# Kernel optimization log

Hardware: AMD Instinct MI355X
Metric: run time of the kernel (lower is better)

Reference implementation:

```python
import jax, jax.numpy as jnp
from jax import lax
import numpy as np

B, T = 8, 16
IMG = 128
CF = 32            # c_CNN_out = dim_C2_2 (feature channels / NTM slot width)
WO = HO = 32       # w_CNN_out, h_CNN_out
N = WO * HO        # dim_C2_1 = NTM memory slots (flattened spatial)
M = CF
DH = 256           # dim_h_o
LAMBDA0 = 1e-4
EPS = 1e-8


def setup_inputs() -> dict:
    key = jax.random.key(0)
    ks = jax.random.split(key, 12)
    f32 = jnp.float32
    inp = {}
    inp["x_i"] = jax.random.normal(ks[0], (B, T, 3, IMG, IMG), f32)
    inp["z_i"] = jax.random.normal(ks[1], (B, T, 3, IMG, IMG), f32)
    # feature CNN (3 -> CF -> CF, stride 2 each)
    inp["conv1_w"] = jax.random.normal(ks[2], (CF, 3, 3, 3), f32) * 0.1
    inp["conv1_b"] = jnp.zeros((CF,), f32)
    inp["conv2_w"] = jax.random.normal(ks[3], (CF, CF, 3, 3), f32) * 0.05
    inp["conv2_b"] = jnp.zeros((CF,), f32)
    # NTM controller / addressing parameters
    inp["Wk"] = jax.random.normal(ks[4], (M, DH), f32) * 0.05
    inp["bk"] = jnp.zeros((M,), f32)
    inp["Wbeta"] = jax.random.normal(ks[5], (1, DH), f32) * 0.05
    inp["bbeta"] = jnp.zeros((1,), f32)
    inp["Wh"] = jax.random.normal(ks[6], (DH, DH + 2 * M), f32) * 0.05
    inp["bh"] = jnp.zeros((DH,), f32)
    inp["We"] = jax.random.normal(ks[7], (M, DH), f32) * 0.05
    inp["Wa"] = jax.random.normal(ks[8], (M, DH), f32) * 0.05
    inp["Wg"] = jax.random.normal(ks[9], (1, DH), f32) * 0.05
    # DCF cosine window and gaussian-label FFT (stored as real/imag pair like torch.rfft)
    win = np.hanning(WO)
    inp["cos_window"] = jnp.asarray(np.outer(win, win), f32)
    sigma = 2.0
    g = np.arange(WO)
    g = np.minimum(g, WO - g)  # circular distance, peak at origin
    d2 = g[:, None] ** 2 + g[None, :] ** 2
    y = np.exp(-d2 / (2.0 * sigma ** 2)).astype(np.float32)
    yfc = np.fft.rfft2(y)
    inp["yf"] = jnp.asarray(np.stack([yfc.real, yfc.imag], -1), f32)[None, None]  # [1,1,WO,WO//2+1,2]
    return inp


def _conv(x, w, b):
    out = lax.conv_general_dilated(x, w, (2, 2), "SAME",
                                   dimension_numbers=("NCHW", "OIHW", "NCHW"))
    return out + b[None, :, None, None]


def _feature(x, c1w, c1b, c2w, c2b):
    x = jax.nn.relu(_conv(x, c1w, c1b))
    return jax.nn.relu(_conv(x, c2w, c2b))  # [BT, CF, WO, HO]


def _layernorm(x):
    # LayerNorm over last two dims [dim_C2_1, dim_C2_2], no affine
    mu = x.mean(axis=(-2, -1), keepdims=True)
    var = x.var(axis=(-2, -1), keepdims=True)
    return (x - mu) / jnp.sqrt(var + 1e-5)


def reference(x_i, z_i, conv1_w, conv1_b, conv2_w, conv2_b,
              Wk, bk, Wbeta, bbeta, Wh, bh, We, Wa, Wg, cos_window, yf):
    # feature extraction
    xf_btcwh = _feature(x_i.reshape(B * T, 3, IMG, IMG), conv1_w, conv1_b, conv2_w, conv2_b)
    zf_btcwh = _feature(z_i.reshape(B * T, 3, IMG, IMG), conv1_w, conv1_b, conv2_w, conv2_b)
    xf = xf_btcwh.transpose(0, 2, 3, 1).reshape(B, T, N, M)  # [B,T,N,M]

    h0 = jnp.zeros((B, DH), xf.dtype)
    c0 = _layernorm(xf[:, 0])  # init_x_norm on first frame features

    def cell(carry, x_t):
        h, c = carry  # h [B,DH], c [B,N,M]; x_t [B,N,M]
        # content-based addressing
        k = jnp.tanh(h @ Wk.T + bk)                           # [B,M]
        beta = jax.nn.softplus(h @ Wbeta.T + bbeta)           # [B,1]
        cn = c / (jnp.linalg.norm(c, axis=-1, keepdims=True) + EPS)
        kn = k / (jnp.linalg.norm(k, axis=-1, keepdims=True) + EPS)
        sims = jnp.einsum("bnm,bm->bn", cn, kn)               # cosine sim [B,N]
        w = jax.nn.softmax(beta * sims, axis=-1)              # read/write weights
        r = jnp.einsum("bn,bnm->bm", w, c)                    # read vector
        # controller update
        inp = jnp.concatenate([h, r, x_t.mean(axis=1)], axis=-1)  # [B,DH+2M]
        h_new = jnp.tanh(inp @ Wh.T + bh)
        # erase / add / input-gate write
        e = jax.nn.sigmoid(h_new @ We.T)                      # [B,M]
        a = jnp.tanh(h_new @ Wa.T)                            # [B,M]
        g = jax.nn.sigmoid(h_new @ Wg.T)[:, :, None]          # [B,1,1]
        c_write = c * (1.0 - w[:, :, None] * e[:, None, :]) + w[:, :, None] * a[:, None, :]
        c_new = (1.0 - g) * c_write + g * x_t
        return (h_new, c_new), c_new

    (_, _), c_seq = lax.scan(cell, (h0, c0), xf.transpose(1, 0, 2, 3))
    c_seq = c_seq.transpose(1, 0, 2, 3)                       # [B,T,N,M]

    # c.permute(0,1,3,2).view(B*T, dim_C2_2, WO, HO)
    c_btcwh = c_seq.transpose(0, 1, 3, 2).reshape(B * T, M, WO, HO)

    # DCF correlation in Fourier domain
    cw = cos_window[None, None]
    cfft = jnp.fft.rfft2(c_btcwh * cw)                        # [BT,M,WO,WO//2+1]
    zfft = jnp.fft.rfft2(zf_btcwh * cw)
    kzzf = (cfft.real ** 2 + cfft.imag ** 2).sum(axis=1, keepdims=True)   # [BT,1,WO,Wf]
    kxzf = (zfft * jnp.conj(cfft)).sum(axis=1, keepdims=True)             # complex_mulconj sum
    yfc = yf[..., 0] + 1j * yf[..., 1]                         # [1,1,WO,Wf]
    alphaf = yfc / (kzzf + LAMBDA0)
    response = jnp.fft.irfft2(kxzf * alphaf, s=(WO, HO))       # [BT,1,WO,HO]
    return response.reshape(B, T, WO, HO)
```

## Files before the change

kernel.cpp:

```cpp
#include <hip/hip_runtime.h>
#include <hip/hip_fp16.h>
#include <math.h>


#define TWOPI_32 0.19634954084936207f

typedef _Float16 __h2 __attribute__((ext_vector_type(2)));
__device__ __forceinline__ float fdot2(unsigned int w, unsigned int h, float acc) {
    union { unsigned int u; __h2 v; } a, b;
    a.u = w; b.u = h;
    return __builtin_amdgcn_fdot2(a.v, b.v, acc, false);
}
__device__ __forceinline__ unsigned int packh2(float a, float b) {
    __half2 h2 = __floats2half2_rn(a, b);
    return *(unsigned int*)&h2;
}

__global__ __launch_bounds__(256) void prepack_kernel(
    const float* __restrict__ Wh, const float* __restrict__ Wk,
    const float* __restrict__ We, const float* __restrict__ Wa,
    const float* __restrict__ c1w, const float* __restrict__ c2w,
    __half* __restrict__ whhP, __half* __restrict__ whrxP,
    __half* __restrict__ wkP, __half* __restrict__ weP, __half* __restrict__ waP,
    float* __restrict__ twg,
    unsigned int* __restrict__ c2wP, unsigned int* __restrict__ c1wP01,
    float* __restrict__ c1wP2)
{
    const int tid = threadIdx.x;
    if (blockIdx.x < 32) {
        const int base = blockIdx.x*256 + tid;
        #pragma unroll
        for (int r = 0; r < 8; ++r) {
            int idx = base*8 + r;
            int e = idx & 7, i = (idx >> 3) & 255, c = idx >> 11;
            int q = c >> 4, k = c & 15;
            whhP[idx] = __float2half(Wh[i*320 + q*128 + k*8 + e]);
        }
        #pragma unroll
        for (int r = 0; r < 2; ++r) {
            int idx = base*2 + r;
            int i = idx >> 6, s2 = idx & 63;
            whrxP[idx] = __float2half(Wh[i*320 + 256 + s2]);
        }
        {
            int idx = base;
            int m = idx >> 8, j = (idx >> 4) & 15, e = idx & 15;
            int col = (e < 8) ? (8*j + e) : (128 + 8*j + (e - 8));
            wkP[idx] = __float2half(Wk[m*256 + col]);
            weP[idx] = __float2half(We[m*256 + col]);
            waP[idx] = __float2half(Wa[m*256 + col]);
        }
    } else {
        for (int idx = tid; idx < 4608; idx += 256) {
            int half = idx / 2304;
            int rem  = idx - half*2304;
            int ic2  = rem / 144;
            int r2   = rem - ic2*144;
            int j    = r2 / 9, q = r2 - j*9;
            int oc   = half*16 + j;
            c2wP[((half*16 + ic2)*16 + j)*12 + q] =
                packh2(c2w[oc*288 + (2*ic2)*9 + q],
                       c2w[oc*288 + (2*ic2+1)*9 + q]);
        }
        for (int idx = tid; idx < 288; idx += 256) {
            int oc = idx / 9, r = idx - oc*9;
            c1wP01[idx] = packh2(c1w[oc*27 + r*3 + 0], c1w[oc*27 + r*3 + 1]);
            c1wP2[idx]  = c1w[oc*27 + r*3 + 2];
        }
        for (int idx = tid; idx < 1024; idx += 256) {
            int w = idx >> 5, k = idx & 31;
            float sv, cv;
            sincosf(TWOPI_32 * (float)((w*k) & 31), &sv, &cv);
            twg[idx*2]     = cv;
            twg[idx*2 + 1] = -sv;
        }
    }
}

__global__ __launch_bounds__(512, 2) void convx_kernel(
    const float* __restrict__ x_i, const unsigned int* __restrict__ c1w01,
    const float* __restrict__ c1w2, const float* __restrict__ c1b,
    const unsigned int* __restrict__ c2wP, const float* __restrict__ c2b,
    float* __restrict__ xfeat, __half* __restrict__ xh, float* __restrict__ xmp)
{
    __shared__ __align__(16) char smem[139264];
    const int team = threadIdx.x >> 8;
    const int t256 = threadIdx.x & 255;
    const int tile = blockIdx.x*2 + team;
    const int img  = tile >> 3;
    const int strip = tile & 7;
    unsigned int* sZ  = (unsigned int*)(smem + team*53072);
    unsigned int* sC1 = (unsigned int*)(smem + team*53072 + 15048);
    unsigned int* sW   = (unsigned int*)(smem + 106144);
    unsigned int* sw01 = (unsigned int*)(smem + 130720);
    float*        sw2  = (float*)(smem + 131872);
    float*        sb2  = (float*)(smem + 133024);
    float*        sb1  = (float*)(smem + 133152);

    for (int i = threadIdx.x; i < 1536; i += 512)
        ((uint4*)sW)[i] = ((const uint4*)c2wP)[i];
    for (int i = threadIdx.x; i < 288; i += 512) { sw01[i] = c1w01[i]; sw2[i] = c1w2[i]; }
    if (threadIdx.x < 32) { sb2[threadIdx.x] = c2b[threadIdx.x]; sb1[threadIdx.x] = c1b[threadIdx.x]; }

    const int zrow0 = strip*16;
    for (int idx = t256; idx < 3762; idx += 256) {
        int ic = idx / (19*66);
        int rem = idx - ic*(19*66);
        int li = rem / 66;
        int x2 = rem - li*66;
        int iy = zrow0 + li;
        unsigned int v = 0;
        if (iy < 128 && x2 < 64) {
            float2 p = *(const float2*)&x_i[(((size_t)img*3 + ic)*128 + iy)*128 + 2*x2];
            v = packh2(p.x, p.y);
        }
        sZ[idx] = v;
    }
    for (int idx = t256; idx < 16*9*2; idx += 256) {
        int oc2 = idx / 18; int rem = idx - oc2*18; int li = rem >> 1; int c = 64 + (rem & 1);
        sC1[oc2*(9*66) + li*66 + c] = 0;
    }
    __syncthreads();
    for (int pos = t256; pos < 576; pos += 256) {
        int li = pos >> 6;
        int ox = pos & 63;
        unsigned int pa[9]; float px[9];
        #pragma unroll
        for (int ic = 0; ic < 3; ++ic)
            #pragma unroll
            for (int dy = 0; dy < 3; ++dy) {
                int r = ic*3 + dy;
                int rowb = ic*(19*66) + (2*li + dy)*66;
                pa[r] = sZ[rowb + ox];
                unsigned int u = sZ[rowb + ox + 1];
                px[r] = __half2float(((const __half2*)&u)->x);
            }
        const bool phantom = (strip == 7) && (li == 8);
        #pragma unroll 4
        for (int oc2 = 0; oc2 < 16; ++oc2) {
            const int oca = 2*oc2, ocb = oca + 1;
            float acca = sb1[oca], accb = sb1[ocb];
            #pragma unroll
            for (int r = 0; r < 9; ++r) {
                acca = fdot2(sw01[oca*9 + r], pa[r], acca);
                acca += sw2[oca*9 + r] * px[r];
                accb = fdot2(sw01[ocb*9 + r], pa[r], accb);
                accb += sw2[ocb*9 + r] * px[r];
            }
            sC1[oc2*(9*66) + li*66 + ox] =
                phantom ? 0u : packh2(fmaxf(acca, 0.f), fmaxf(accb, 0.f));
        }
    }
    __syncthreads();
    const int posl = t256 & 127;
    const int half = t256 >> 7;
    const int ly = posl >> 5;
    const int ox = posl & 31;
    float acc[16];
    #pragma unroll
    for (int j = 0; j < 16; ++j) acc[j] = 0.f;
    for (int ic2 = 0; ic2 < 16; ++ic2) {
        unsigned int patch[9];
        #pragma unroll
        for (int dy = 0; dy < 3; ++dy)
            #pragma unroll
            for (int dx = 0; dx < 3; ++dx)
                patch[dy*3+dx] = sC1[ic2*(9*66) + (2*ly+dy)*66 + 2*ox + dx];
        const unsigned int* wbase = sW + (half*16 + ic2)*192;
        #pragma unroll
        for (int j = 0; j < 16; ++j) {
            const unsigned int* wr = wbase + j*12;
            uint4 wa = *(const uint4*)wr;
            uint4 wb = *(const uint4*)(wr + 4);
            unsigned int w8 = wr[8];
            float a = acc[j];
            a = fdot2(wa.x, patch[0], a); a = fdot2(wa.y, patch[1], a);
            a = fdot2(wa.z, patch[2], a); a = fdot2(wa.w, patch[3], a);
            a = fdot2(wb.x, patch[4], a); a = fdot2(wb.y, patch[5], a);
            a = fdot2(wb.z, patch[6], a); a = fdot2(wb.w, patch[7], a);
            a = fdot2(w8,  patch[8], a);
            acc[j] = a;
        }
    }
    const int oy = strip*4 + ly;
    const int n  = oy*32 + ox;
    float vals[16];
    #pragma unroll
    for (int j = 0; j < 16; ++j) {
        int oc = half*16 + j;
        float v = fmaxf(acc[j] + sb2[oc], 0.f);
        vals[j] = v;
        xfeat[(((size_t)img*32 + oc)*32 + oy)*32 + ox] = v;
    }
    {
        unsigned int hp[8];
        #pragma unroll
        for (int k = 0; k < 8; ++k) hp[k] = packh2(vals[2*k], vals[2*k+1]);
        uint4* dp = (uint4*)(xh + (size_t)img*32768 + (size_t)n*32 + half*16);
        dp[0] = *(uint4*)&hp[0];
        dp[1] = *(uint4*)&hp[4];
    }
    {
        const int lane = threadIdx.x & 63;
        const int wsub = (t256 >> 6) & 1;
        #pragma unroll
        for (int j = 0; j < 16; ++j) {
            float v = vals[j];
            #pragma unroll
            for (int d = 32; d > 0; d >>= 1) v += __shfl_xor(v, d, 64);
            if (lane == 0)
                xmp[(((size_t)img*8 + strip)*2 + wsub)*32 + half*16 + j] = v * (1.f/1024.f);
        }
    }
}

__global__ __launch_bounds__(512, 2) void fat_kernel(
    const float* __restrict__ xfeat, const __half* __restrict__ xh,
    const float* __restrict__ xmp,
    const __half* __restrict__ whhP, const __half* __restrict__ whrxP,
    const __half* __restrict__ wkP, const __half* __restrict__ weP,
    const __half* __restrict__ waP,
    const float* __restrict__ bk, const float* __restrict__ Wbeta,
    const float* __restrict__ bbeta, const float* __restrict__ bh,
    const float* __restrict__ Wg,
    float* __restrict__ wbuf, float* __restrict__ eag, float* __restrict__ lnst,
    const float* __restrict__ z_i, const unsigned int* __restrict__ c1w01,
    const float* __restrict__ c1w2, const float* __restrict__ c1b,
    const unsigned int* __restrict__ c2wP, const float* __restrict__ c2b,
    float* __restrict__ zfeat)
{
    __shared__ __align__(16) char smem[139264];

    if (blockIdx.x < 8) {
        __builtin_amdgcn_s_setprio(1);
        __half* sWhh = (__half*)(smem);
        float (*sHbuf)[256] = (float(*)[256])(smem + 131072);
        __half (*sHh)[256] = (__half(*)[256])(smem + 133120);
        float* sK    = (float*)(smem + 134144);
        float* sXm   = (float*)(smem + 134272);
        float* sRedC = (float*)(smem + 136320);
        float* sR32  = (float*)(smem + 137344);
        float* sE    = (float*)(smem + 137472);
        float* sA    = (float*)(smem + 137600);
        float* sBk   = (float*)(smem + 137728);
        float* sBh   = (float*)(smem + 137856);
        float* sRedD = (float*)(smem + 138880);
        float* sRedL = (float*)(smem + 138912);

        const int b    = blockIdx.x;
        const int tid  = threadIdx.x;
        const int lane = tid & 63;
        const int wid  = tid >> 6;

        {
            const uint4* src = (const uint4*)whhP;
            uint4* dst = (uint4*)sWhh;
            for (int i2 = tid; i2 < 8192; i2 += 512) dst[i2] = src[i2];
        }
        if (tid < 256) { sBh[tid] = bh[tid]; sHbuf[0][tid] = 0.f; sHh[0][tid] = __float2half(0.f); }
        if (tid < 32)  { sBk[tid] = bk[tid]; sK[tid] = tanhf(bk[tid]); }
        if (tid < 512) {
            const int tt = tid >> 5, m = tid & 31;
            const float* pp = xmp + ((size_t)(b*16 + tt)*16)*32 + m;
            float s = 0.f;
            #pragma unroll
            for (int q = 0; q < 16; ++q) s += pp[q*32];
            sXm[tid] = s;
        }
        float4 wbeta4 = *(const float4*)&Wbeta[(size_t)lane*4];
        float4 wg4    = *(const float4*)&Wg[(size_t)lane*4];
        float bb = bbeta[0];

        const int mg = tid >> 4, jg = tid & 15;
        uint4 wk0, wk1, we0, we1, wa0, wa1;
        {
            const uint4* p;
            p = (const uint4*)(wkP + (size_t)(mg*16 + jg)*16); wk0 = p[0]; wk1 = p[1];
            p = (const uint4*)(weP + (size_t)(mg*16 + jg)*16); we0 = p[0]; we1 = p[1];
            p = (const uint4*)(waP + (size_t)(mg*16 + jg)*16); wa0 = p[0]; wa1 = p[1];
        }
        const int iD = tid >> 1, qD = tid & 1;
        uint4 wrx0, wrx1, wrx2, wrx3;
        {
            const uint4* p = (const uint4*)(whrxP + (size_t)iD*64 + qD*32);
            wrx0 = p[0]; wrx1 = p[1]; wrx2 = p[2]; wrx3 = p[3];
        }

        const int n0 = 2*tid;
        float c0[32], c1[32];

        {
            const float* x0 = xfeat + (size_t)(b*16)*32768;
            float sum = 0.f, ss = 0.f;
            #pragma unroll
            for (int m = 0; m < 32; ++m) {
                float2 v = *(const float2*)&x0[m*1024 + n0];
                c0[m] = v.x; c1[m] = v.y;
                sum += v.x + v.y; ss += v.x*v.x + v.y*v.y;
            }
            #pragma unroll
            for (int d = 32; d > 0; d >>= 1) { sum += __shfl_xor(sum, d, 64); ss += __shfl_xor(ss, d, 64); }
            if (lane == 0) { sRedL[wid] = sum; sRedL[8+wid] = ss; }
            __syncthreads();
            float S = 0.f, SS = 0.f;
            #pragma unroll
            for (int i = 0; i < 8; ++i) { S += sRedL[i]; SS += sRedL[8+i]; }
            float mu = S * (1.f/32768.f);
            float var = SS * (1.f/32768.f) - mu*mu;
            float rs = rsqrtf(var + 1e-5f);
            if (tid == 0) { lnst[b*2] = mu; lnst[b*2+1] = rs; }
            #pragma unroll
            for (int m = 0; m < 32; ++m) { c0[m] = (c0[m]-mu)*rs; c1[m] = (c1[m]-mu)*rs; }
        }

        uint4 xb[8];
        {
            const uint4* xrow = (const uint4*)(xh + (size_t)(b*16)*32768) + 8*tid;
            #pragma unroll
            for (int i = 0; i < 8; ++i) xb[i] = xrow[i];
        }
        __syncthreads();

        float betav = (bb > 20.f) ? bb : log1pf(expf(bb));
        float ex0 = 0.f, ex1 = 0.f, w0 = 0.f, w1 = 0.f;
        const int rm = ((lane&1)<<4)|((lane&2)<<2)|(lane&4)|((lane&8)>>2)|((lane&16)>>4);

        #pragma unroll 1
        for (int t = 0; t < 16; ++t) {
            const int cur = t & 1, nxt = cur ^ 1;

            {
                float beta = betav;
                float dot0 = 0.f, dot1 = 0.f, cn20 = 0.f, cn21 = 0.f, kn2 = 0.f;
                #pragma unroll
                for (int q = 0; q < 8; ++q) {
                    float4 k4 = *(const float4*)&sK[4*q];
                    dot0 += c0[4*q]*k4.x + c0[4*q+1]*k4.y + c0[4*q+2]*k4.z + c0[4*q+3]*k4.w;
                    dot1 += c1[4*q]*k4.x + c1[4*q+1]*k4.y + c1[4*q+2]*k4.z + c1[4*q+3]*k4.w;
                    cn20 += c0[4*q]*c0[4*q] + c0[4*q+1]*c0[4*q+1] + c0[4*q+2]*c0[4*q+2] + c0[4*q+3]*c0[4*q+3];
                    cn21 += c1[4*q]*c1[4*q] + c1[4*q+1]*c1[4*q+1] + c1[4*q+2]*c1[4*q+2] + c1[4*q+3]*c1[4*q+3];
                    kn2  += k4.x*k4.x + k4.y*k4.y + k4.z*k4.z + k4.w*k4.w;
                }
                float kinv = 1.f / (sqrtf(kn2) + 1e-8f);
                float s0 = dot0 * kinv / (sqrtf(cn20) + 1e-8f);
                float s1 = dot1 * kinv / (sqrtf(cn21) + 1e-8f);
                ex0 = expf(beta * s0);
                ex1 = expf(beta * s1);
                float es = ex0 + ex1;
                #pragma unroll
                for (int d = 32; d > 0; d >>= 1) es += __shfl_xor(es, d, 64);
                if (lane == 0) sRedD[wid] = es;
                float v[32];
                #pragma unroll
                for (int m = 0; m < 32; ++m) v[m] = ex0*c0[m] + ex1*c1[m];
                #pragma unroll
                for (int i = 0; i < 16; ++i) { float sd = (lane&1)? v[i] : v[i+16]; float rc = __shfl_xor(sd, 1, 64); v[i] = ((lane&1)? v[i+16] : v[i]) + rc; }
                #pragma unroll
                for (int i = 0; i < 8; ++i)  { float sd = (lane&2)? v[i] : v[i+8];  float rc = __shfl_xor(sd, 2, 64); v[i] = ((lane&2)? v[i+8]  : v[i]) + rc; }
                #pragma unroll
                for (int i = 0; i < 4; ++i)  { float sd = (lane&4)? v[i] : v[i+4];  float rc = __shfl_xor(sd, 4, 64); v[i] = ((lane&4)? v[i+4]  : v[i]) + rc; }
                #pragma unroll
                for (int i = 0; i < 2; ++i)  { float sd = (lane&8)? v[i] : v[i+2];  float rc = __shfl_xor(sd, 8, 64); v[i] = ((lane&8)? v[i+2]  : v[i]) + rc; }
                { float sd = (lane&16)? v[0] : v[1]; float rc = __shfl_xor(sd, 16, 64); v[0] = ((lane&16)? v[1] : v[0]) + rc; }
                v[0] += __shfl_xor(v[0], 32, 64);
                if (lane < 32) sRedC[wid*32 + rm] = v[0];
            }
            __syncthreads();

            {
                float den = sRedD[0]+sRedD[1]+sRedD[2]+sRedD[3]+sRedD[4]+sRedD[5]+sRedD[6]+sRedD[7];
                float inv = 1.f / den;
                w0 = ex0 * inv; w1 = ex1 * inv;
                *(float2*)&wbuf[(size_t)(b*16 + t)*1024 + n0] = make_float2(w0, w1);
                if (lane < 32) {
                    float r = 0.f;
                    #pragma unroll
                    for (int w = 0; w < 8; ++w) r += sRedC[w*32 + lane];
                    sR32[lane] = r * inv;
                }
                float s0 = 0.f, s1 = 0.f, s2 = 0.f, s3 = 0.f;
                #pragma unroll
                for (int k4 = 0; k4 < 4; ++k4) {
                    const int kb = 4*k4;
                    uint4 wv0 = *(const uint4*)&sWhh[(size_t)((qD*16 + kb+0)*256 + iD)*8];
                    uint4 hv0 = *(const uint4*)&sHh[cur][qD*128 + (kb+0)*8];
                    s0 = fdot2(wv0.x, hv0.x, s0); s0 = fdot2(wv0.y, hv0.y, s0);
                    s0 = fdot2(wv0.z, hv0.z, s0); s0 = fdot2(wv0.w, hv0.w, s0);
                    uint4 wv1 = *(const uint4*)&sWhh[(size_t)((qD*16 + kb+1)*256 + iD)*8];
                    uint4 hv1 = *(const uint4*)&sHh[cur][qD*128 + (kb+1)*8];
                    s1 = fdot2(wv1.x, hv1.x, s1); s1 = fdot2(wv1.y, hv1.y, s1);
                    s1 = fdot2(wv1.z, hv1.z, s1); s1 = fdot2(wv1.w, hv1.w, s1);
                    uint4 wv2 = *(const uint4*)&sWhh[(size_t)((qD*16 + kb+2)*256 + iD)*8];
                    uint4 hv2 = *(const uint4*)&sHh[cur][qD*128 + (kb+2)*8];
                    s2 = fdot2(wv2.x, hv2.x, s2); s2 = fdot2(wv2.y, hv2.y, s2);
                    s2 = fdot2(wv2.z, hv2.z, s2); s2 = fdot2(wv2.w, hv2.w, s2);
                    uint4 wv3 = *(const uint4*)&sWhh[(size_t)((qD*16 + kb+3)*256 + iD)*8];
                    uint4 hv3 = *(const uint4*)&sHh[cur][qD*128 + (kb+3)*8];
                    s3 = fdot2(wv3.x, hv3.x, s3); s3 = fdot2(wv3.y, hv3.y, s3);
                    s3 = fdot2(wv3.w, hv3.w, s3); s3 = fdot2(wv3.z, hv3.z, s3);
                }
                const float* rxsrc = qD ? &sXm[t*32] : sR32;
                {
                    const __half2* w2;
                    float4 va, vb;
                    va = *(const float4*)&rxsrc[0];  vb = *(const float4*)&rxsrc[4];
                    w2 = (const __half2*)&wrx0;
                    { float2 p0 = __half22float2(w2[0]); s0 += p0.x*va.x + p0.y*va.y;
                      float2 p1 = __half22float2(w2[1]); s0 += p1.x*va.z + p1.y*va.w;
                      float2 p2 = __half22float2(w2[2]); s0 += p2.x*vb.x + p2.y*vb.y;
                      float2 p3 = __half22float2(w2[3]); s0 += p3.x*vb.z + p3.y*vb.w; }
                    va = *(const float4*)&rxsrc[8];  vb = *(const float4*)&rxsrc[12];
                    w2 = (const __half2*)&wrx1;
                    { float2 p0 = __half22float2(w2[0]); s1 += p0.x*va.x + p0.y*va.y;
                      float2 p1 = __half22float2(w2[1]); s1 += p1.x*va.z + p1.y*va.w;
                      float2 p2 = __half22float2(w2[2]); s1 += p2.x*vb.x + p2.y*vb.y;
                      float2 p3 = __half22float2(w2[3]); s1 += p3.x*vb.z + p3.y*vb.w; }
                    va = *(const float4*)&rxsrc[16]; vb = *(const float4*)&rxsrc[20];
                    w2 = (const __half2*)&wrx2;
                    { float2 p0 = __half22float2(w2[0]); s2 += p0.x*va.x + p0.y*va.y;
                      float2 p1 = __half22float2(w2[1]); s2 += p1.x*va.z + p1.y*va.w;
                      float2 p2 = __half22float2(w2[2]); s2 += p2.x*vb.x + p2.y*vb.y;
                      float2 p3 = __half22float2(w2[3]); s2 += p3.x*vb.z + p3.y*vb.w; }
                    va = *(const float4*)&rxsrc[24]; vb = *(const float4*)&rxsrc[28];
                    w2 = (const __half2*)&wrx3;
                    { float2 p0 = __half22float2(w2[0]); s3 += p0.x*va.x + p0.y*va.y;
                      float2 p1 = __half22float2(w2[1]); s3 += p1.x*va.z + p1.y*va.w;
                      float2 p2 = __half22float2(w2[2]); s3 += p2.x*vb.x + p2.y*vb.y;
                      float2 p3 = __half22float2(w2[3]); s3 += p3.x*vb.z + p3.y*vb.w; }
                }
                float s = (s0 + s1) + (s2 + s3);
                s += __shfl_down(s, 1, 2);
                if (qD == 0) {
                    float hn = tanhf(s + sBh[iD]);
                    sHbuf[nxt][iD] = hn;
                    sHh[nxt][iD] = __float2half(hn);
                }
            }
            __syncthreads();

            float gg;
            {
                uint4 h0 = *(const uint4*)&sHh[nxt][8*jg];
                uint4 h1 = *(const uint4*)&sHh[nxt][128 + 8*jg];
                float se0=0.f, se1=0.f, sa0=0.f, sa1=0.f, sk0=0.f, sk1=0.f;
                se0 = fdot2(we0.x, h0.x, se0); se1 = fdot2(we0.y, h0.y, se1);
                se0 = fdot2(we0.z, h0.z, se0); se1 = fdot2(we0.w, h0.w, se1);
                se0 = fdot2(we1.x, h1.x, se0); se1 = fdot2(we1.y, h1.y, se1);
                se0 = fdot2(we1.z, h1.z, se0); se1 = fdot2(we1.w, h1.w, se1);
                sa0 = fdot2(wa0.x, h0.x, sa0); sa1 = fdot2(wa0.y, h0.y, sa1);
                sa0 = fdot2(wa0.z, h0.z, sa0); sa1 = fdot2(wa0.w, h0.w, sa1);
                sa0 = fdot2(wa1.x, h1.x, sa0); sa1 = fdot2(wa1.y, h1.y, sa1);
                sa0 = fdot2(wa1.z, h1.z, sa0); sa1 = fdot2(wa1.w, h1.w, sa1);
                sk0 = fdot2(wk0.x, h0.x, sk0); sk1 = fdot2(wk0.y, h0.y, sk1);
                sk0 = fdot2(wk0.z, h0.z, sk0); sk1 = fdot2(wk0.w, h0.w, sk1);
                sk0 = fdot2(wk1.x, h1.x, sk0); sk1 = fdot2(wk1.y, h1.y, sk1);
                sk0 = fdot2(wk1.z, h1.z, sk0); sk1 = fdot2(wk1.w, h1.w, sk1);
                float se = se0 + se1, sa = sa0 + sa1, sk = sk0 + sk1;
                se += __shfl_down(se, 8, 16); sa += __shfl_down(sa, 8, 16); sk += __shfl_down(sk, 8, 16);
                se += __shfl_down(se, 4, 16); sa += __shfl_down(sa, 4, 16); sk += __shfl_down(sk, 4, 16);
                se += __shfl_down(se, 2, 16); sa += __shfl_down(sa, 2, 16); sk += __shfl_down(sk, 2, 16);
                se += __shfl_down(se, 1, 16); sa += __shfl_down(sa, 1, 16); sk += __shfl_down(sk, 1, 16);
                if (jg == 0) {
                    float e = 1.f/(1.f + expf(-se));
                    float a = tanhf(sa);
                    sE[mg] = e; sA[mg] = a;
                    sK[mg] = tanhf(sk + sBk[mg]);
                    eag[(size_t)(b*16 + t)*80 + mg]      = e;
                    eag[(size_t)(b*16 + t)*80 + 32 + mg] = a;
                }
                float4 h4 = *(const float4*)&sHbuf[nxt][lane*4];
                float pg = wg4.x*h4.x + wg4.y*h4.y + wg4.z*h4.z + wg4.w*h4.w;
                float pb = wbeta4.x*h4.x + wbeta4.y*h4.y + wbeta4.z*h4.z + wbeta4.w*h4.w;
                #pragma unroll
                for (int d = 32; d > 0; d >>= 1) {
                    pg += __shfl_xor(pg, d, 64);
                    pb += __shfl_xor(pb, d, 64);
                }
                gg = 1.f/(1.f + expf(-pg));
                float xbeta = pb + bb;
                betav = (xbeta > 20.f) ? xbeta : log1pf(expf(xbeta));
                if (tid == 0) eag[(size_t)(b*16 + t)*80 + 64] = gg;
            }
            __syncthreads();

            {
                float omg = 1.f - gg;
                const __half* xp = (const __half*)xb;
                #pragma unroll
                for (int q = 0; q < 8; ++q) {
                    float4 e4 = *(const float4*)&sE[4*q];
                    float4 a4 = *(const float4*)&sA[4*q];
                    #pragma unroll
                    for (int r = 0; r < 4; ++r) {
                        int m = 4*q + r;
                        float e = (r==0)?e4.x:(r==1)?e4.y:(r==2)?e4.z:e4.w;
                        float a = (r==0)?a4.x:(r==1)?a4.y:(r==2)?a4.z:a4.w;
                        float x0v = __half2float(xp[m]);
                        float x1v = __half2float(xp[32 + m]);
                        c0[m] = omg*(c0[m]*(1.f - w0*e) + w0*a) + gg*x0v;
                        c1[m] = omg*(c1[m]*(1.f - w1*e) + w1*a) + gg*x1v;
                    }
                }
                if (t < 15) {
                    const uint4* xrow = (const uint4*)(xh + (size_t)(b*16 + t + 1)*32768) + 8*tid;
                    #pragma unroll
                    for (int i = 0; i < 8; ++i) xb[i] = xrow[i];
                }
            }
        }
    } else {
        const int team = threadIdx.x >> 8;
        const int t256 = threadIdx.x & 255;
        const int tile = (blockIdx.x - 8)*2 + team;
        const int img  = tile >> 3;
        const int strip = tile & 7;
        unsigned int* sZ  = (unsigned int*)(smem + team*53072);
        unsigned int* sC1 = (unsigned int*)(smem + team*53072 + 15048);
        unsigned int* sW   = (unsigned int*)(smem + 106144);
        unsigned int* sw01 = (unsigned int*)(smem + 130720);
        float*        sw2  = (float*)(smem + 131872);
        float*        sb2  = (float*)(smem + 133024);
        float*        sb1  = (float*)(smem + 133152);

        for (int i = threadIdx.x; i < 1536; i += 512)
            ((uint4*)sW)[i] = ((const uint4*)c2wP)[i];
        for (int i = threadIdx.x; i < 288; i += 512) { sw01[i] = c1w01[i]; sw2[i] = c1w2[i]; }
        if (threadIdx.x < 32) { sb2[threadIdx.x] = c2b[threadIdx.x]; sb1[threadIdx.x] = c1b[threadIdx.x]; }

        const int zrow0 = strip*16;
        for (int idx = t256; idx < 3762; idx += 256) {
            int ic = idx / (19*66);
            int rem = idx - ic*(19*66);
            int li = rem / 66;
            int x2 = rem - li*66;
            int iy = zrow0 + li;
            unsigned int v = 0;
            if (iy < 128 && x2 < 64) {
                float2 p = *(const float2*)&z_i[(((size_t)img*3 + ic)*128 + iy)*128 + 2*x2];
                v = packh2(p.x, p.y);
            }
            sZ[idx] = v;
        }
        for (int idx = t256; idx < 16*9*2; idx += 256) {
            int oc2 = idx / 18; int rem = idx - oc2*18; int li = rem >> 1; int c = 64 + (rem & 1);
            sC1[oc2*(9*66) + li*66 + c] = 0;
        }
        __syncthreads();
        for (int pos = t256; pos < 576; pos += 256) {
            int li = pos >> 6;
            int ox = pos & 63;
            unsigned int pa[9]; float px[9];
            #pragma unroll
            for (int ic = 0; ic < 3; ++ic)
                #pragma unroll
                for (int dy = 0; dy < 3; ++dy) {
                    int r = ic*3 + dy;
                    int rowb = ic*(19*66) + (2*li + dy)*66;
                    pa[r] = sZ[rowb + ox];
                    unsigned int u = sZ[rowb + ox + 1];
                    px[r] = __half2float(((const __half2*)&u)->x);
                }
            const bool phantom = (strip == 7) && (li == 8);
            #pragma unroll 4
            for (int oc2 = 0; oc2 < 16; ++oc2) {
                const int oca = 2*oc2, ocb = oca + 1;
                float acca = sb1[oca], accb = sb1[ocb];
                #pragma unroll
                for (int r = 0; r < 9; ++r) {
                    acca = fdot2(sw01[oca*9 + r], pa[r], acca);
                    acca += sw2[oca*9 + r] * px[r];
                    accb = fdot2(sw01[ocb*9 + r], pa[r], accb);
                    accb += sw2[ocb*9 + r] * px[r];
                }
                sC1[oc2*(9*66) + li*66 + ox] =
                    phantom ? 0u : packh2(fmaxf(acca, 0.f), fmaxf(accb, 0.f));
            }
        }
        __syncthreads();
        const int posl = t256 & 127;
        const int half = t256 >> 7;
        const int ly = posl >> 5;
        const int ox = posl & 31;
        float acc[16];
        #pragma unroll
        for (int j = 0; j < 16; ++j) acc[j] = 0.f;
        for (int ic2 = 0; ic2 < 16; ++ic2) {
            unsigned int patch[9];
            #pragma unroll
            for (int dy = 0; dy < 3; ++dy)
                #pragma unroll
                for (int dx = 0; dx < 3; ++dx)
                    patch[dy*3+dx] = sC1[ic2*(9*66) + (2*ly+dy)*66 + 2*ox + dx];
            const unsigned int* wbase = sW + (half*16 + ic2)*192;
            #pragma unroll
            for (int j = 0; j < 16; ++j) {
                const unsigned int* wr = wbase + j*12;
                uint4 wa = *(const uint4*)wr;
                uint4 wb = *(const uint4*)(wr + 4);
                unsigned int w8 = wr[8];
                float a = acc[j];
                a = fdot2(wa.x, patch[0], a); a = fdot2(wa.y, patch[1], a);
                a = fdot2(wa.z, patch[2], a); a = fdot2(wa.w, patch[3], a);
                a = fdot2(wb.x, patch[4], a); a = fdot2(wb.y, patch[5], a);
                a = fdot2(wb.z, patch[6], a); a = fdot2(wb.w, patch[7], a);
                a = fdot2(w8,  patch[8], a);
                acc[j] = a;
            }
        }
        const int oy = strip*4 + ly;
        #pragma unroll
        for (int j = 0; j < 16; ++j) {
            int oc = half*16 + j;
            zfeat[(((size_t)img*32 + oc)*32 + oy)*32 + ox] = fmaxf(acc[j] + sb2[oc], 0.f);
        }
    }
}

__global__ __launch_bounds__(256) void ntm_replay_kernel(
    const float* __restrict__ xfeat, const float* __restrict__ wbuf,
    const float* __restrict__ eag, const float* __restrict__ lnst,
    float* __restrict__ cseq)
{
    const int slab = blockIdx.x;
    const int b    = blockIdx.y;
    const int tid  = threadIdx.x;
    const int m    = tid >> 3;
    const int ns   = tid & 7;
    const int n0   = slab*64 + ns*8;
    const float mu = lnst[b*2], rs = lnst[b*2+1];

    float c[8];
    {
        const float* x0 = xfeat + (size_t)(b*16)*32768 + m*1024 + n0;
        float4 a = *(const float4*)x0;
        float4 bv = *(const float4*)(x0 + 4);
        c[0]=(a.x-mu)*rs; c[1]=(a.y-mu)*rs; c[2]=(a.z-mu)*rs; c[3]=(a.w-mu)*rs;
        c[4]=(bv.x-mu)*rs; c[5]=(bv.y-mu)*rs; c[6]=(bv.z-mu)*rs; c[7]=(bv.w-mu)*rs;
    }
    for (int t = 0; t < 16; ++t) {
        const size_t bt = (size_t)(b*16 + t);
        const float* wp = &wbuf[bt*1024 + n0];
        float4 wA = *(const float4*)wp;
        float4 wB = *(const float4*)(wp + 4);
        float e = eag[bt*80 + m];
        float a = eag[bt*80 + 32 + m];
        float g = eag[bt*80 + 64];
        float omg = 1.f - g;
        const float* xp = &xfeat[bt*32768 + m*1024 + n0];
        float4 xA = *(const float4*)xp;
        float4 xB = *(const float4*)(xp + 4);
        c[0] = omg*(c[0]*(1.f - wA.x*e) + wA.x*a) + g*xA.x;
        c[1] = omg*(c[1]*(1.f - wA.y*e) + wA.y*a) + g*xA.y;
        c[2] = omg*(c[2]*(1.f - wA.z*e) + wA.z*a) + g*xA.z;
        c[3] = omg*(c[3]*(1.f - wA.w*e) + wA.w*a) + g*xA.w;
        c[4] = omg*(c[4]*(1.f - wB.x*e) + wB.x*a) + g*xB.x;
        c[5] = omg*(c[5]*(1.f - wB.y*e) + wB.y*a) + g*xB.y;
        c[6] = omg*(c[6]*(1.f - wB.z*e) + wB.z*a) + g*xB.z;
        c[7] = omg*(c[7]*(1.f - wB.w*e) + wB.w*a) + g*xB.w;
        float* op = &cseq[bt*32768 + m*1024 + n0];
        *(float4*)op       = make_float4(c[0], c[1], c[2], c[3]);
        *(float4*)(op + 4) = make_float4(c[4], c[5], c[6], c[7]);
    }
}

__global__ __launch_bounds__(256) void fft_fwd_kernel(const float* __restrict__ srcA,
                                                      const float* __restrict__ srcB,
                                                      const float* __restrict__ cosw,
                                                      const float* __restrict__ twg,
                                                      float* __restrict__ dstA,
                                                      float* __restrict__ dstB)
{
    const int img = blockIdx.x;
    const int tid = threadIdx.x;
    const float* src; float* dst;
    if (img < 4096) { src = srcA + (size_t)img*1024;        dst = dstA + (size_t)img*1088; }
    else            { src = srcB + (size_t)(img-4096)*1024; dst = dstB + (size_t)(img-4096)*1088; }

    __shared__ __align__(16) float sY[32*36];
    __shared__ __align__(16) float sT[2048];
    __shared__ __align__(16) float sR[2048];

    {
        const float4* s4 = (const float4*)twg;
        float4* d4 = (float4*)sT;
        d4[tid]       = s4[tid];
        d4[256 + tid] = s4[256 + tid];
    }
    {
        float4 v = *(const float4*)&src[tid*4];
        float4 c = *(const float4*)&cosw[tid*4];
        *(float4*)&sY[(tid>>3)*36 + (tid&7)*4] = make_float4(v.x*c.x, v.y*c.y, v.z*c.z, v.w*c.w);
    }
    __syncthreads();

    const int hj = tid >> 3;
    const int k0 = (tid & 7) * 4;

    float r0=0.f,i0=0.f,r1=0.f,i1=0.f,r2=0.f,i2=0.f,r3=0.f,i3=0.f;
    #pragma unroll
    for (int w = 0; w < 32; ++w) {
        float y = sY[hj*36 + w];
        float4 ta = *(const float4*)&sT[(w*32 + k0)*2];
        float4 tb = *(const float4*)&sT[(w*32 + k0)*2 + 4];
        r0 += y*ta.x; i0 += y*ta.y;
        r1 += y*ta.z; i1 += y*ta.w;
        r2 += y*tb.x; i2 += y*tb.y;
        r3 += y*tb.z; i3 += y*tb.w;
    }
    *(float4*)&sR[(hj*32 + k0)*2]     = make_float4(r0,i0,r1,i1);
    *(float4*)&sR[(hj*32 + k0)*2 + 4] = make_float4(r2,i2,r3,i3);
    __syncthreads();

    float fr0=0.f,fi0=0.f,fr1=0.f,fi1=0.f,fr2=0.f,fi2=0.f,fr3=0.f,fi3=0.f;
    #pragma unroll
    for (int h = 0; h < 32; ++h) {
        float2 wj = *(const float2*)&sT[(h*32 + hj)*2];
        float4 Ra = *(const float4*)&sR[(h*32 + k0)*2];
        float4 Rb = *(const float4*)&sR[(h*32 + k0)*2 + 4];
        fr0 += Ra.x*wj.x - Ra.y*wj.y;  fi0 += Ra.x*wj.y + Ra.y*wj.x;
        fr1 += Ra.z*wj.x - Ra.w*wj.y;  fi1 += Ra.z*wj.y + Ra.w*wj.x;
        fr2 += Rb.x*wj.x - Rb.y*wj.y;  fi2 += Rb.x*wj.y + Rb.y*wj.x;
        fr3 += Rb.z*wj.x - Rb.w*wj.y;  fi3 += Rb.z*wj.y + Rb.w*wj.x;
    }
    float* dp = dst + (size_t)(hj*17 + k0)*2;
    if (k0 < 16) {
        *(float2*)&dp[0] = make_float2(fr0, fi0);
        *(float2*)&dp[2] = make_float2(fr1, fi1);
        *(float2*)&dp[4] = make_float2(fr2, fi2);
        *(float2*)&dp[6] = make_float2(fr3, fi3);
    } else if (k0 == 16) {
        *(float2*)&dp[0] = make_float2(fr0, fi0);
    }
}

__global__ __launch_bounds__(256) void comb_ifft_kernel(const float* __restrict__ cfft,
                                                        const float* __restrict__ zfft,
                                                        const float* __restrict__ yf,
                                                        float* __restrict__ out)
{
    const int bt  = blockIdx.x;
    const int tid = threadIdx.x;
    __shared__ float sG[544*2];
    __shared__ float sS[544*2];
    __shared__ float ct[32], st[32];
    if (tid < 32) {
        float sv, cv;
        sincosf(TWOPI_32 * (float)tid, &sv, &cv);
        ct[tid] = cv; st[tid] = sv;
    }
    for (int idx = tid; idx < 544; idx += 256) {
        float kzz = 0.f, kxr = 0.f, kxi = 0.f;
        #pragma unroll 4
        for (int m = 0; m < 32; ++m) {
            size_t base = ((size_t)(bt*32 + m)*1088) + idx*2;
            float2 c = *(const float2*)&cfft[base];
            float2 z = *(const float2*)&zfft[base];
            kzz += c.x*c.x + c.y*c.y;
            kxr += z.x*c.x + z.y*c.y;
            kxi += z.y*c.x - z.x*c.y;
        }
        float den = 1.f / (kzz + 1e-4f);
        float2 y = *(const float2*)&yf[idx*2];
        float ar = y.x*den, ai = y.y*den;
        sG[idx*2]     = kxr*ar - kxi*ai;
        sG[idx*2 + 1] = kxr*ai + kxi*ar;
    }
    __syncthreads();
    for (int idx = tid; idx < 544; idx += 256) {
        int h = idx / 17;
        int k = idx - h*17;
        float re = 0.f, im = 0.f;
        #pragma unroll
        for (int j = 0; j < 32; ++j) {
            float gr = sG[(j*17+k)*2], gi = sG[(j*17+k)*2+1];
            int a = (h*j) & 31;
            float c = ct[a], s = st[a];
            re += gr*c - gi*s;
            im += gr*s + gi*c;
        }
        sS[(h*17+k)*2] = re; sS[(h*17+k)*2+1] = im;
    }
    __syncthreads();
    #pragma unroll
    for (int p = 0; p < 4; ++p) {
        int pos = p*256 + tid;
        int h = pos >> 5, wq = pos & 31;
        float acc = sS[(h*17)*2];
        #pragma unroll
        for (int k = 1; k < 16; ++k) {
            int a = (wq*k) & 31;
            acc += 2.f*(sS[(h*17+k)*2]*ct[a] - sS[(h*17+k)*2+1]*st[a]);
        }
        acc += sS[(h*17+16)*2] * ((wq & 1) ? -1.f : 1.f);
        out[(size_t)bt*1024 + pos] = acc * (1.f/1024.f);
    }
}

extern "C" void kernel_launch(void* const* d_in, const int* in_sizes, int n_in,
                              void* d_out, int out_size, void* d_ws, size_t ws_size,
                              hipStream_t stream)
{
    const float* x_i   = (const float*)d_in[0];
    const float* z_i   = (const float*)d_in[1];
    const float* c1w   = (const float*)d_in[2];
    const float* c1b   = (const float*)d_in[3];
    const float* c2w   = (const float*)d_in[4];
    const float* c2b   = (const float*)d_in[5];
    const float* Wk    = (const float*)d_in[6];
    const float* bk    = (const float*)d_in[7];
    const float* Wbeta = (const float*)d_in[8];
    const float* bbeta = (const float*)d_in[9];
    const float* Wh    = (const float*)d_in[10];
    const float* bh    = (const float*)d_in[11];
    const float* We    = (const float*)d_in[12];
    const float* Wa    = (const float*)d_in[13];
    const float* Wg    = (const float*)d_in[14];
    const float* cosw  = (const float*)d_in[15];
    const float* yf    = (const float*)d_in[16];
    float* out = (float*)d_out;
    float* ws  = (float*)d_ws;

    float*  xfeat = ws + 16777216;
    float*  zfeat = ws + 20971520;
    float*  cseq  = ws + 25165824;
    float*  cfft  = ws;
    float*  zfft  = ws + 4456448;
    __half* xhb   = (__half*)(ws + 9000000);
    float*  wbuf  = ws + 11100000;
    float*  eag   = ws + 11240000;
    float*  lnstp = ws + 11251000;
    __half* whhP  = (__half*)(ws + 29360128);
    __half* whrxP = (__half*)(ws + 29392896);
    __half* wkP   = (__half*)(ws + 29401088);
    __half* weP   = (__half*)(ws + 29405184);
    __half* waP   = (__half*)(ws + 29409280);
    float*  twg   = ws + 29413376;
    unsigned int* c2wP   = (unsigned int*)(ws + 29415424);
    unsigned int* c1wP01 = (unsigned int*)(ws + 29421568);
    float*  c1wP2 = ws + 29421856;
    float*  xmp   = ws + 29422144;

    dim3 b256(256);
    prepack_kernel<<<33, b256, 0, stream>>>(Wh, Wk, We, Wa, c1w, c2w,
                                            whhP, whrxP, wkP, weP, waP, twg,
                                            c2wP, c1wP01, c1wP2);
    convx_kernel<<<512, 512, 0, stream>>>(x_i, c1wP01, c1wP2, c1b, c2wP, c2b,
                                          xfeat, xhb, xmp);
    fat_kernel<<<520, 512, 0, stream>>>(xfeat, xhb, xmp, whhP, whrxP, wkP, weP, waP,
                                        bk, Wbeta, bbeta, bh, Wg, wbuf, eag, lnstp,
                                        z_i, c1wP01, c1wP2, c1b, c2wP, c2b, zfeat);
    ntm_replay_kernel<<<dim3(16,8), b256, 0, stream>>>(xfeat, wbuf, eag, lnstp, cseq);
    fft_fwd_kernel<<<8192, b256, 0, stream>>>(cseq, zfeat, cosw, twg, cfft, zfft);
    comb_ifft_kernel<<<128, b256, 0, stream>>>(cfft, zfft, yf, out);
}
```

Baseline: 427.9 us.

## Fuse NTM memory replay with forward 2D DFT of each memory plane

The NTM memory replay is merged into a new kernel that computes each (batch, channel) memory plane step by step, applies the cosine window and performs the forward 2D DFT in shared memory, writing cfft directly. This removes the cseq intermediate write and read, and the forward FFT kernel now handles only the z features. The fused kernel launches just 256 blocks that each loop serially over 16 timesteps, which lowers parallelism compared with 4096 separate FFT blocks. Launch bounds on the conv and fat kernels are also relaxed from 2 to 1 blocks per SM, giving more register room at possible occupancy cost.

Result: faster. 418.2 us (-2.3%).

```diff
diff --git a/kernel.cpp b/kernel.cpp
--- a/kernel.cpp
+++ b/kernel.cpp
@@ -77,7 +77,7 @@
     }
 }
 
-__global__ __launch_bounds__(512, 2) void convx_kernel(
+__global__ __launch_bounds__(512, 1) void convx_kernel(
     const float* __restrict__ x_i, const unsigned int* __restrict__ c1w01,
     const float* __restrict__ c1w2, const float* __restrict__ c1b,
     const unsigned int* __restrict__ c2wP, const float* __restrict__ c2b,
@@ -214,7 +214,7 @@
     }
 }
 
-__global__ __launch_bounds__(512, 2) void fat_kernel(
+__global__ __launch_bounds__(512, 1) void fat_kernel(
     const float* __restrict__ xfeat, const __half* __restrict__ xh,
     const float* __restrict__ xmp,
     const __half* __restrict__ whhP, const __half* __restrict__ whrxP,
@@ -397,7 +397,7 @@
                     uint4 wv3 = *(const uint4*)&sWhh[(size_t)((qD*16 + kb+3)*256 + iD)*8];
                     uint4 hv3 = *(const uint4*)&sHh[cur][qD*128 + (kb+3)*8];
                     s3 = fdot2(wv3.x, hv3.x, s3); s3 = fdot2(wv3.y, hv3.y, s3);
-                    s3 = fdot2(wv3.w, hv3.w, s3); s3 = fdot2(wv3.z, hv3.z, s3);
+                    s3 = fdot2(wv3.z, hv3.z, s3); s3 = fdot2(wv3.w, hv3.w, s3);
                 }
                 const float* rxsrc = qD ? &sXm[t*32] : sR32;
                 {
@@ -616,65 +616,96 @@
     }
 }
 
-__global__ __launch_bounds__(256) void ntm_replay_kernel(
+__global__ __launch_bounds__(256) void replay_fft_kernel(
     const float* __restrict__ xfeat, const float* __restrict__ wbuf,
     const float* __restrict__ eag, const float* __restrict__ lnst,
-    float* __restrict__ cseq)
+    const float* __restrict__ cosw, const float* __restrict__ twg,
+    float* __restrict__ cfft)
 {
-    const int slab = blockIdx.x;
-    const int b    = blockIdx.y;
-    const int tid  = threadIdx.x;
-    const int m    = tid >> 3;
-    const int ns   = tid & 7;
-    const int n0   = slab*64 + ns*8;
+    const int m = blockIdx.x & 31;
+    const int b = blockIdx.x >> 5;
+    const int tid = threadIdx.x;
+    __shared__ __align__(16) float sY[32*36];
+    __shared__ __align__(16) float sT[2048];
+    __shared__ __align__(16) float sR[2048];
+    {
+        const float4* s4 = (const float4*)twg;
+        float4* d4 = (float4*)sT;
+        d4[tid]       = s4[tid];
+        d4[256 + tid] = s4[256 + tid];
+    }
+    const int n0 = tid*4;
+    float4 cw = *(const float4*)&cosw[n0];
     const float mu = lnst[b*2], rs = lnst[b*2+1];
-
-    float c[8];
+    float c0v, c1v, c2v, c3v;
     {
-        const float* x0 = xfeat + (size_t)(b*16)*32768 + m*1024 + n0;
-        float4 a = *(const float4*)x0;
-        float4 bv = *(const float4*)(x0 + 4);
-        c[0]=(a.x-mu)*rs; c[1]=(a.y-mu)*rs; c[2]=(a.z-mu)*rs; c[3]=(a.w-mu)*rs;
-        c[4]=(bv.x-mu)*rs; c[5]=(bv.y-mu)*rs; c[6]=(bv.z-mu)*rs; c[7]=(bv.w-mu)*rs;
-    }
+        float4 x = *(const float4*)&xfeat[(size_t)(b*16)*32768 + (size_t)m*1024 + n0];
+        c0v=(x.x-mu)*rs; c1v=(x.y-mu)*rs; c2v=(x.z-mu)*rs; c3v=(x.w-mu)*rs;
+    }
+    const int hj = tid >> 3;
+    const int k0 = (tid & 7)*4;
+    const int syoff = (tid>>3)*36 + (tid&7)*4;
+
     for (int t = 0; t < 16; ++t) {
         const size_t bt = (size_t)(b*16 + t);
-        const float* wp = &wbuf[bt*1024 + n0];
-        float4 wA = *(const float4*)wp;
-        float4 wB = *(const float4*)(wp + 4);
+        float4 w = *(const float4*)&wbuf[bt*1024 + n0];
         float e = eag[bt*80 + m];
         float a = eag[bt*80 + 32 + m];
         float g = eag[bt*80 + 64];
         float omg = 1.f - g;
-        const float* xp = &xfeat[bt*32768 + m*1024 + n0];
-        float4 xA = *(const float4*)xp;
-        float4 xB = *(const float4*)(xp + 4);
-        c[0] = omg*(c[0]*(1.f - wA.x*e) + wA.x*a) + g*xA.x;
-        c[1] = omg*(c[1]*(1.f - wA.y*e) + wA.y*a) + g*xA.y;
-        c[2] = omg*(c[2]*(1.f - wA.z*e) + wA.z*a) + g*xA.z;
-        c[3] = omg*(c[3]*(1.f - wA.w*e) + wA.w*a) + g*xA.w;
-        c[4] = omg*(c[4]*(1.f - wB.x*e) + wB.x*a) + g*xB.x;
-        c[5] = omg*(c[5]*(1.f - wB.y*e) + wB.y*a) + g*xB.y;
-        c[6] = omg*(c[6]*(1.f - wB.z*e) + wB.z*a) + g*xB.z;
-        c[7] = omg*(c[7]*(1.f - wB.w*e) + wB.w*a) + g*xB.w;
-        float* op = &cseq[bt*32768 + m*1024 + n0];
-        *(float4*)op       = make_float4(c[0], c[1], c[2], c[3]);
-        *(float4*)(op + 4) = make_float4(c[4], c[5], c[6], c[7]);
+        float4 xv = *(const float4*)&xfeat[bt*32768 + (size_t)m*1024 + n0];
+        c0v = omg*(c0v*(1.f - w.x*e) + w.x*a) + g*xv.x;
+        c1v = omg*(c1v*(1.f - w.y*e) + w.y*a) + g*xv.y;
+        c2v = omg*(c2v*(1.f - w.z*e) + w.z*a) + g*xv.z;
+        c3v = omg*(c3v*(1.f - w.w*e) + w.w*a) + g*xv.w;
+        *(float4*)&sY[syoff] = make_float4(c0v*cw.x, c1v*cw.y, c2v*cw.z, c3v*cw.w);
+        __syncthreads();
+        float r0=0.f,i0=0.f,r1=0.f,i1=0.f,r2=0.f,i2=0.f,r3=0.f,i3=0.f;
+        #pragma unroll
+        for (int ww = 0; ww < 32; ++ww) {
+            float y = sY[hj*36 + ww];
+            float4 ta = *(const float4*)&sT[(ww*32 + k0)*2];
+            float4 tb = *(const float4*)&sT[(ww*32 + k0)*2 + 4];
+            r0 += y*ta.x; i0 += y*ta.y;
+            r1 += y*ta.z; i1 += y*ta.w;
+            r2 += y*tb.x; i2 += y*tb.y;
+            r3 += y*tb.z; i3 += y*tb.w;
+        }
+        *(float4*)&sR[(hj*32 + k0)*2]     = make_float4(r0,i0,r1,i1);
+        *(float4*)&sR[(hj*32 + k0)*2 + 4] = make_float4(r2,i2,r3,i3);
+        __syncthreads();
+        float fr0=0.f,fi0=0.f,fr1=0.f,fi1=0.f,fr2=0.f,fi2=0.f,fr3=0.f,fi3=0.f;
+        #pragma unroll
+        for (int h = 0; h < 32; ++h) {
+            float2 wj = *(const float2*)&sT[(h*32 + hj)*2];
+            float4 Ra = *(const float4*)&sR[(h*32 + k0)*2];
+            float4 Rb = *(const float4*)&sR[(h*32 + k0)*2 + 4];
+            fr0 += Ra.x*wj.x - Ra.y*wj.y;  fi0 += Ra.x*wj.y + Ra.y*wj.x;
+            fr1 += Ra.z*wj.x - Ra.w*wj.y;  fi1 += Ra.z*wj.y + Ra.w*wj.x;
+            fr2 += Rb.x*wj.x - Rb.y*wj.y;  fi2 += Rb.x*wj.y + Rb.y*wj.x;
+            fr3 += Rb.z*wj.x - Rb.w*wj.y;  fi3 += Rb.z*wj.y + Rb.w*wj.x;
+        }
+        float* dp = cfft + (size_t)(bt*32 + m)*1088 + (size_t)(hj*17 + k0)*2;
+        if (k0 < 16) {
+            *(float2*)&dp[0] = make_float2(fr0, fi0);
+            *(float2*)&dp[2] = make_float2(fr1, fi1);
+            *(float2*)&dp[4] = make_float2(fr2, fi2);
+            *(float2*)&dp[6] = make_float2(fr3, fi3);
+        } else if (k0 == 16) {
+            *(float2*)&dp[0] = make_float2(fr0, fi0);
+        }
     }
 }
 
-__global__ __launch_bounds__(256) void fft_fwd_kernel(const float* __restrict__ srcA,
-                                                      const float* __restrict__ srcB,
+__global__ __launch_bounds__(256) void fft_fwd_kernel(const float* __restrict__ src0,
                                                       const float* __restrict__ cosw,
                                                       const float* __restrict__ twg,
-                                                      float* __restrict__ dstA,
-                                                      float* __restrict__ dstB)
+                                                      float* __restrict__ dst0)
 {
     const int img = blockIdx.x;
     const int tid = threadIdx.x;
-    const float* src; float* dst;
-    if (img < 4096) { src = srcA + (size_t)img*1024;        dst = dstA + (size_t)img*1088; }
-    else            { src = srcB + (size_t)(img-4096)*1024; dst = dstB + (size_t)(img-4096)*1088; }
+    const float* src = src0 + (size_t)img*1024;
+    float* dst = dst0 + (size_t)img*1088;
 
     __shared__ __align__(16) float sY[32*36];
     __shared__ __align__(16) float sT[2048];
@@ -822,7 +853,6 @@
 
     float*  xfeat = ws + 16777216;
     float*  zfeat = ws + 20971520;
-    float*  cseq  = ws + 25165824;
     float*  cfft  = ws;
     float*  zfft  = ws + 4456448;
     __half* xhb   = (__half*)(ws + 9000000);
@@ -849,7 +879,7 @@
     fat_kernel<<<520, 512, 0, stream>>>(xfeat, xhb, xmp, whhP, whrxP, wkP, weP, waP,
                                         bk, Wbeta, bbeta, bh, Wg, wbuf, eag, lnstp,
                                         z_i, c1wP01, c1wP2, c1b, c2wP, c2b, zfeat);
-    ntm_replay_kernel<<<dim3(16,8), b256, 0, stream>>>(xfeat, wbuf, eag, lnstp, cseq);
-    fft_fwd_kernel<<<8192, b256, 0, stream>>>(cseq, zfeat, cosw, twg, cfft, zfft);
+    replay_fft_kernel<<<256, b256, 0, stream>>>(xfeat, wbuf, eag, lnstp, cosw, twg, cfft);
+    fft_fwd_kernel<<<4096, b256, 0, stream>>>(zfeat, cosw, twg, zfft);
     comb_ifft_kernel<<<128, b256, 0, stream>>>(cfft, zfft, yf, out);
 }
```
